# Performance work log

Measured on AMD Instinct MI355X. Metric: run time of the kernel, lower is better.

Reference implementation:

```python
import jax, jax.numpy as jnp
import numpy as np

DIM, NH = 256, 8
B, L_INNER, L_LEAF, L_ROOT = 16, 128, 64, 16


def mha(q, k, v, wi, bi, wo, bo, nh=NH):
    # Faithful torch.nn.MultiheadAttention (batch_first): packed in_proj, q scaled by head_dim**-0.5.
    E = q.shape[-1]
    hd = E // nh
    wq, wk, wv = wi[:E], wi[E:2 * E], wi[2 * E:]
    bq, bk, bv = bi[:E], bi[E:2 * E], bi[2 * E:]

    def proj(x, w, b):
        Bx, Lx, _ = x.shape
        return (x @ w.T + b).reshape(Bx, Lx, nh, hd).transpose(0, 2, 1, 3)  # [B,H,L,hd]

    qh = proj(q, wq, bq) * (float(hd) ** -0.5)
    kh = proj(k, wk, bk)
    vh = proj(v, wv, bv)
    attn = jax.nn.softmax(jnp.einsum('bhqd,bhkd->bhqk', qh, kh), axis=-1)
    o = jnp.einsum('bhqk,bhkd->bhqd', attn, vh).transpose(0, 2, 1, 3).reshape(q.shape)
    return o @ wo.T + bo


def setup_inputs() -> dict:
    key = jax.random.key(0)
    ks = jax.random.split(key, 10)
    return {
        'leaf': jax.random.normal(ks[0], (B * L_INNER, L_LEAF, DIM), jnp.float32),
        'inner': jax.random.normal(ks[1], (B, L_INNER, DIM), jnp.float32),
        'root': jax.random.normal(ks[2], (B, L_ROOT, DIM), jnp.float32),
        'w_in': jax.random.normal(ks[3], (7, 3 * DIM, DIM), jnp.float32) * 0.02,
        'b_in': jax.random.normal(ks[4], (7, 3 * DIM), jnp.float32) * 0.02,
        'w_out': jax.random.normal(ks[5], (7, DIM, DIM), jnp.float32) * 0.02,
        'b_out': jax.random.normal(ks[6], (7, DIM), jnp.float32) * 0.02,
        'weight_leaf': jax.random.normal(ks[7], (2,), jnp.float32),
        'weight_inner': jax.random.normal(ks[8], (3,), jnp.float32),
        'weight_root': jax.random.normal(ks[9], (2,), jnp.float32),
    }


def reference(leaf, inner, root, w_in, b_in, w_out, b_out, weight_leaf, weight_inner, weight_root):
    # param slots: 0 leaf_parents, 1 leaf_siblings, 2 inner_parents, 3 inner_siblings,
    #              4 inner_children, 5 root_siblings, 6 root_children (constructed but UNUSED, as in source)
    inner_flat = inner.reshape(-1, 1, DIM)  # [B*L_inner, 1, dim]

    leaf_p = mha(leaf, inner_flat, inner_flat, w_in[0], b_in[0], w_out[0], b_out[0])
    leaf_s = mha(leaf, leaf, leaf, w_in[1], b_in[1], w_out[1], b_out[1])
    wl = jax.nn.softmax(weight_leaf)
    leaf_out = wl[0] * leaf_p + wl[1] * leaf_s

    inner_p = mha(inner, root, root, w_in[2], b_in[2], w_out[2], b_out[2])
    inner_s = mha(inner, inner, inner, w_in[3], b_in[3], w_out[3], b_out[3])
    inner_c = mha(inner_flat, leaf, leaf, w_in[4], b_in[4], w_out[4], b_out[4]).reshape(inner.shape)
    wi_ = jax.nn.softmax(weight_inner)
    inner_out = wi_[0] * inner_p + wi_[1] * inner_s + wi_[2] * inner_c

    root_s = mha(root, root, root, w_in[5], b_in[5], w_out[5], b_out[5])
    # source bug reproduced: root_c also uses attn_root_siblings (slot 5)
    root_c = mha(root, inner, inner, w_in[5], b_in[5], w_out[5], b_out[5])
    wr = jax.nn.softmax(weight_root)
    root_out = wr[0] * root_s + wr[1] * root_c

    return (leaf_out, inner_out, root_out)
```

## Files before the change

kernel.cpp:

```cpp
#include <hip/hip_runtime.h>
#include <hip/hip_bf16.h>
#include <cstdint>


#define DIM 256
#define NH 8
#define HD 32

static constexpr float SCALE = 0.17677669529663687f;

typedef __bf16 bf16x8 __attribute__((ext_vector_type(8)));
typedef __bf16 bf16x4 __attribute__((ext_vector_type(4)));
typedef float  f32x4  __attribute__((ext_vector_type(4)));

__device__ __forceinline__ float dot4(const float4 a, const float4 b) {
    return a.x * b.x + a.y * b.y + a.z * b.z + a.w * b.w;
}

__device__ __forceinline__ void cvt_range(const float* __restrict__ s,
                                          __bf16* __restrict__ d, int lb, int n) {
    int i = (lb * 256 + (int)threadIdx.x) * 4;
    if (i < n) {
        float4 v = *(const float4*)(s + i);
        d[i + 0] = (__bf16)v.x; d[i + 1] = (__bf16)v.y;
        d[i + 2] = (__bf16)v.z; d[i + 3] = (__bf16)v.w;
    }
}

__global__ __launch_bounds__(256) void cvt_all(
    const float* __restrict__ w_in, const float* __restrict__ w_out,
    __bf16* __restrict__ W1b, __bf16* __restrict__ W4kvb,
    __bf16* __restrict__ Wo1b, __bf16* __restrict__ Wv0b,
    __bf16* __restrict__ Wo0b)
{
    const size_t WI = 768 * 256, WO = 256 * 256;
    const int bid = blockIdx.x;
    if (bid < 192)       cvt_range(w_in + 1 * WI, W1b, bid, 768 * 256);
    else if (bid < 320)  cvt_range(w_in + 4 * WI + 256 * 256, W4kvb, bid - 192, 512 * 256);
    else if (bid < 384)  cvt_range(w_out + 1 * WO, Wo1b, bid - 320, 256 * 256);
    else if (bid < 448)  cvt_range(w_in + 512 * 256, Wv0b, bid - 384, 256 * 256);
    else                 cvt_range(w_out, Wo0b, bid - 448, 256 * 256);
}

__device__ void mega2_body(int g,
    const float* __restrict__ X, const float* __restrict__ inner,
    const __bf16* __restrict__ W1b, const float* __restrict__ Bi1,
    const __bf16* __restrict__ W4kvb, const float* __restrict__ W4q,
    const float* __restrict__ Bi4, __bf16* __restrict__ O1,
    float* __restrict__ Oc, char* __restrict__ smem)
{
    const int xcd  = g & 7;
    const int idx  = g >> 3;
    const int b    = xcd * 256 + (idx >> 2);
    const int hg   = idx & 3;
    const int tid  = threadIdx.x;
    const int wid  = tid >> 6;
    const int lane = tid & 63;
    const int lr   = lane & 15;
    const int lk   = (lane >> 4) * 8;
    const int prow = (lane >> 4) * 4;

    __bf16* Xs  = (__bf16*)smem;
    __bf16* Qs  = (__bf16*)smem;
    __bf16* Pw  = (__bf16*)(smem + wid * 2304);
    __bf16* Ks  = (__bf16*)(smem + 9216);
    __bf16* K4t = (__bf16*)(smem + 18432);
    float* qpart = (float*)(smem + 27648);
    float* qv    = qpart + 256;
    float* psm   = qv + 64;
    float* opart = psm + 128;
    __bf16* Vt  = (__bf16*)(smem + 33792);
    __bf16* V4t = (__bf16*)(smem + 43008);

    {
        const float* xb = X + (size_t)b * 64 * DIM;
#pragma unroll
        for (int it = 0; it < 16; ++it) {
            const int e4 = it * 1024 + tid * 4;
            const f32x4 v = __builtin_nontemporal_load((const f32x4*)(xb + e4));
            bf16x4 t4;
            t4[0] = (__bf16)v[0]; t4[1] = (__bf16)v[1];
            t4[2] = (__bf16)v[2]; t4[3] = (__bf16)v[3];
            const int row = e4 >> 8, col = e4 & 255;
            *(bf16x4*)(Xs + row * 264 + col) = t4;
        }
    }
    __syncthreads();

    bf16x8 af[4][8];
#pragma unroll
    for (int tg = 0; tg < 4; ++tg)
#pragma unroll
        for (int kk = 0; kk < 8; ++kk)
            af[tg][kk] = *(const bf16x8*)(Xs + (size_t)(tg * 16 + lr) * 264 + kk * 32 + lk);
    __syncthreads();

    {
        auto wsrc = [&](int t) -> const __bf16* {
            if (t < 12) {
                const int sec = t >> 2, sub = t & 3;
                return W1b + (size_t)(sec * 256 + hg * 64 + sub * 16) * DIM;
            }
            const int u = t - 12, sec = u >> 2, sub = u & 3;
            return W4kvb + (size_t)(sec * 256 + hg * 64 + sub * 16) * DIM;
        };
        const size_t boff = (size_t)lr * DIM + lk;
        const int t0w = wid * 5;
        bf16x8 bw[8], bn[8];
        {
            const __bf16* p = wsrc(t0w) + boff;
#pragma unroll
            for (int kk = 0; kk < 8; ++kk) bw[kk] = *(const bf16x8*)(p + kk * 32);
        }
        for (int i = 0; i < 5; ++i) {
            const int t = t0w + i;
            if (i + 1 < 5) {
                const __bf16* p = wsrc(t + 1) + boff;
#pragma unroll
                for (int kk = 0; kk < 8; ++kk) bn[kk] = *(const bf16x8*)(p + kk * 32);
            }
            f32x4 acc0 = {0.f,0.f,0.f,0.f}, acc1 = {0.f,0.f,0.f,0.f};
            f32x4 acc2 = {0.f,0.f,0.f,0.f}, acc3 = {0.f,0.f,0.f,0.f};
#pragma unroll
            for (int kk = 0; kk < 8; ++kk) {
                acc0 = __builtin_amdgcn_mfma_f32_16x16x32_bf16(af[0][kk], bw[kk], acc0, 0, 0, 0);
                acc1 = __builtin_amdgcn_mfma_f32_16x16x32_bf16(af[1][kk], bw[kk], acc1, 0, 0, 0);
                acc2 = __builtin_amdgcn_mfma_f32_16x16x32_bf16(af[2][kk], bw[kk], acc2, 0, 0, 0);
                acc3 = __builtin_amdgcn_mfma_f32_16x16x32_bf16(af[3][kk], bw[kk], acc3, 0, 0, 0);
            }
            f32x4 accT[4] = { acc0, acc1, acc2, acc3 };
            const int sub = t & 3;
            const int col = sub * 16 + lr;
            if (t < 4) {
                const float bias = Bi1[hg * 64 + sub * 16 + lr];
#pragma unroll
                for (int tg = 0; tg < 4; ++tg)
#pragma unroll
                    for (int r = 0; r < 4; ++r)
                        Qs[(size_t)(tg * 16 + prow + r) * 72 + col] =
                            (__bf16)((accT[tg][r] + bias) * SCALE);
            } else if (t < 8) {
                const float bias = Bi1[256 + hg * 64 + sub * 16 + lr];
#pragma unroll
                for (int tg = 0; tg < 4; ++tg)
#pragma unroll
                    for (int r = 0; r < 4; ++r)
                        Ks[(size_t)(tg * 16 + prow + r) * 72 + col] =
                            (__bf16)(accT[tg][r] + bias);
            } else if (t < 12) {
                const float bias = Bi1[512 + hg * 64 + sub * 16 + lr];
#pragma unroll
                for (int tg = 0; tg < 4; ++tg) {
                    bf16x4 pv;
#pragma unroll
                    for (int r = 0; r < 4; ++r) pv[r] = (__bf16)(accT[tg][r] + bias);
                    *(bf16x4*)(Vt + (size_t)col * 72 + tg * 16 + prow) = pv;
                }
            } else if (t < 16) {
                const float bias = Bi4[256 + hg * 64 + sub * 16 + lr];
#pragma unroll
                for (int tg = 0; tg < 4; ++tg) {
                    bf16x4 pv;
#pragma unroll
                    for (int r = 0; r < 4; ++r) pv[r] = (__bf16)(accT[tg][r] + bias);
                    *(bf16x4*)(K4t + (size_t)col * 72 + tg * 16 + prow) = pv;
                }
            } else {
                const float bias = Bi4[512 + hg * 64 + sub * 16 + lr];
#pragma unroll
                for (int tg = 0; tg < 4; ++tg) {
                    bf16x4 pv;
#pragma unroll
                    for (int r = 0; r < 4; ++r) pv[r] = (__bf16)(accT[tg][r] + bias);
                    *(bf16x4*)(V4t + (size_t)col * 72 + tg * 16 + prow) = pv;
                }
            }
#pragma unroll
            for (int kk = 0; kk < 8; ++kk) bw[kk] = bn[kk];
        }
    }
    __syncthreads();

    {
        const int o = tid & 63, part = tid >> 6;
        const float4* wr = (const float4*)(W4q + (size_t)(hg * 64 + o) * DIM + part * 64);
        const float4* xr = (const float4*)(inner + (size_t)b * DIM + part * 64);
        float accq = 0.f;
#pragma unroll
        for (int k = 0; k < 16; ++k) accq += dot4(xr[k], wr[k]);
        qpart[part * 64 + o] = accq;
    }
    __syncthreads();

    if (tid < 64)
        qv[tid] = (qpart[tid] + qpart[64 + tid] + qpart[128 + tid] + qpart[192 + tid]
                   + Bi4[hg * 64 + tid]) * SCALE;

    const int hh = wid >> 1;
    const int qh = wid & 1;
    f32x4 s[2][4];
    {
        bf16x8 kb[4];
#pragma unroll
        for (int kt = 0; kt < 4; ++kt)
            kb[kt] = *(const bf16x8*)(Ks + (size_t)(kt * 16 + lr) * 72 + hh * 32 + lk);
#pragma unroll
        for (int q2 = 0; q2 < 2; ++q2) {
            const int qt = qh * 2 + q2;
            const bf16x8 qa = *(const bf16x8*)(Qs + (size_t)(qt * 16 + lr) * 72 + hh * 32 + lk);
#pragma unroll
            for (int kt = 0; kt < 4; ++kt) {
                f32x4 z = {0.f, 0.f, 0.f, 0.f};
                s[q2][kt] = __builtin_amdgcn_mfma_f32_16x16x32_bf16(qa, kb[kt], z, 0, 0, 0);
            }
        }
    }
#pragma unroll
    for (int q2 = 0; q2 < 2; ++q2) {
#pragma unroll
        for (int r = 0; r < 4; ++r) {
            float m = fmaxf(fmaxf(s[q2][0][r], s[q2][1][r]), fmaxf(s[q2][2][r], s[q2][3][r]));
#pragma unroll
            for (int off = 1; off < 16; off <<= 1) m = fmaxf(m, __shfl_xor(m, off));
            const float p0 = __expf(s[q2][0][r] - m), p1 = __expf(s[q2][1][r] - m);
            const float p2 = __expf(s[q2][2][r] - m), p3 = __expf(s[q2][3][r] - m);
            float t = p0 + p1 + p2 + p3;
#pragma unroll
            for (int off = 1; off < 16; off <<= 1) t += __shfl_xor(t, off);
            const float inv = 1.0f / t;
            s[q2][0][r] = p0 * inv; s[q2][1][r] = p1 * inv;
            s[q2][2][r] = p2 * inv; s[q2][3][r] = p3 * inv;
        }
    }
    bf16x8 vb[2][2];
#pragma unroll
    for (int dt = 0; dt < 2; ++dt)
#pragma unroll
        for (int ks = 0; ks < 2; ++ks)
            vb[dt][ks] = *(const bf16x8*)(Vt + (size_t)(hh * 32 + dt * 16 + lr) * 72 + ks * 32 + lk);
    __syncthreads();

    {
#pragma unroll
        for (int q2 = 0; q2 < 2; ++q2) {
            const int qt = qh * 2 + q2;
#pragma unroll
            for (int kt = 0; kt < 4; ++kt)
#pragma unroll
                for (int r = 0; r < 4; ++r)
                    Pw[(size_t)(prow + r) * 72 + kt * 16 + lr] = (__bf16)s[q2][kt][r];
            bf16x8 pa[2];
#pragma unroll
            for (int ks = 0; ks < 2; ++ks)
                pa[ks] = *(const bf16x8*)(Pw + (size_t)lr * 72 + ks * 32 + lk);
#pragma unroll
            for (int dt = 0; dt < 2; ++dt) {
                f32x4 o = {0.f, 0.f, 0.f, 0.f};
#pragma unroll
                for (int ks = 0; ks < 2; ++ks)
                    o = __builtin_amdgcn_mfma_f32_16x16x32_bf16(pa[ks], vb[dt][ks], o, 0, 0, 0);
                const int colO = (hg * 2 + hh) * 32 + dt * 16 + lr;
#pragma unroll
                for (int r = 0; r < 4; ++r)
                    __builtin_nontemporal_store((__bf16)o[r],
                        &O1[((size_t)b * 64 + qt * 16 + prow + r) * DIM + colO]);
            }
        }
    }
    __syncthreads();

    if (wid < 2) {
        const int j = lane;
        float sv = 0.f;
#pragma unroll
        for (int d = 0; d < 32; ++d)
            sv += qv[wid * 32 + d] * (float)K4t[(size_t)(wid * 32 + d) * 72 + j];
        float m = sv;
#pragma unroll
        for (int off = 1; off < 64; off <<= 1) m = fmaxf(m, __shfl_xor(m, off));
        const float p = __expf(sv - m);
        float t = p;
#pragma unroll
        for (int off = 1; off < 64; off <<= 1) t += __shfl_xor(t, off);
        psm[wid * 64 + j] = p / t;
    }
    __syncthreads();

    if (tid < 128) {
        const int o = tid & 63, hf = tid >> 6;
        const int ho = o >> 5;
        float acc2 = 0.f;
#pragma unroll
        for (int j = 0; j < 32; ++j)
            acc2 += psm[ho * 64 + hf * 32 + j] * (float)V4t[(size_t)o * 72 + hf * 32 + j];
        opart[hf * 64 + o] = acc2;
    }
    __syncthreads();
    if (tid < 64)
        Oc[(size_t)b * DIM + hg * 64 + tid] = opart[tid] + opart[64 + tid];
}

__device__ void leafp_mfma_body(int bid, const float* __restrict__ inner,
    const __bf16* __restrict__ Wv0b, const __bf16* __restrict__ Wo0b,
    const float* __restrict__ b_in0, const float* __restrict__ b_out0,
    float* __restrict__ tP, char* __restrict__ smem)
{
    __bf16* tV = (__bf16*)smem;
    __bf16* Bs = (__bf16*)(smem + 33792);
    const int tid  = threadIdx.x;
    const int wid  = tid >> 6;
    const int lane = tid & 63;
    const int lr   = lane & 15;
    const int lk   = (lane >> 4) * 8;
    const int prow = (lane >> 4) * 4;
    const int tok0 = wid * 16 + prow;
    const int srow = tid >> 5;
    const int scol = (tid & 31) * 8;

    bf16x8 a[8];
    {
        const float* xrow = inner + ((size_t)bid * 64 + wid * 16 + lr) * DIM + lk;
#pragma unroll
        for (int k = 0; k < 8; ++k) {
            float4 v0 = *(const float4*)(xrow + k * 32);
            float4 v1 = *(const float4*)(xrow + k * 32 + 4);
            bf16x8 t;
            t[0] = (__bf16)v0.x; t[1] = (__bf16)v0.y; t[2] = (__bf16)v0.z; t[3] = (__bf16)v0.w;
            t[4] = (__bf16)v1.x; t[5] = (__bf16)v1.y; t[6] = (__bf16)v1.z; t[7] = (__bf16)v1.w;
            a[k] = t;
        }
    }

    {
        bf16x8 g0 = *(const bf16x8*)(Wv0b + (size_t)srow * DIM + scol);
        bf16x8 g1 = *(const bf16x8*)(Wv0b + (size_t)(8 + srow) * DIM + scol);
        *(bf16x8*)(Bs + srow * 264 + scol) = g0;
        *(bf16x8*)(Bs + (8 + srow) * 264 + scol) = g1;
    }
    __syncthreads();
    for (int t = 0; t < 16; ++t) {
        const int cur = t & 1;
        const __bf16* Bc = Bs + cur * 4224;
        bf16x8 g0, g1;
        if (t + 1 < 16) {
            const __bf16* p = Wv0b + (size_t)((t + 1) * 16) * DIM;
            g0 = *(const bf16x8*)(p + (size_t)srow * DIM + scol);
            g1 = *(const bf16x8*)(p + (size_t)(8 + srow) * DIM + scol);
        }
        f32x4 acc = {0.f, 0.f, 0.f, 0.f};
#pragma unroll
        for (int k = 0; k < 8; ++k)
            acc = __builtin_amdgcn_mfma_f32_16x16x32_bf16(
                a[k], *(const bf16x8*)(Bc + lr * 264 + k * 32 + lk), acc, 0, 0, 0);
        const float bias = b_in0[512 + t * 16 + lr];
#pragma unroll
        for (int r = 0; r < 4; ++r)
            tV[(size_t)(tok0 + r) * 264 + t * 16 + lr] = (__bf16)(acc[r] + bias);
        if (t + 1 < 16) {
            __bf16* Bn = Bs + (cur ^ 1) * 4224;
            *(bf16x8*)(Bn + srow * 264 + scol) = g0;
            *(bf16x8*)(Bn + (8 + srow) * 264 + scol) = g1;
        }
        __syncthreads();
    }

    bf16x8 a2[8];
#pragma unroll
    for (int k = 0; k < 8; ++k)
        a2[k] = *(const bf16x8*)(tV + (size_t)(wid * 16 + lr) * 264 + k * 32 + lk);
    {
        bf16x8 g0 = *(const bf16x8*)(Wo0b + (size_t)srow * DIM + scol);
        bf16x8 g1 = *(const bf16x8*)(Wo0b + (size_t)(8 + srow) * DIM + scol);
        *(bf16x8*)(Bs + srow * 264 + scol) = g0;
        *(bf16x8*)(Bs + (8 + srow) * 264 + scol) = g1;
    }
    __syncthreads();
    for (int t = 0; t < 16; ++t) {
        const int cur = t & 1;
        const __bf16* Bc = Bs + cur * 4224;
        bf16x8 g0, g1;
        if (t + 1 < 16) {
            const __bf16* p = Wo0b + (size_t)((t + 1) * 16) * DIM;
            g0 = *(const bf16x8*)(p + (size_t)srow * DIM + scol);
            g1 = *(const bf16x8*)(p + (size_t)(8 + srow) * DIM + scol);
        }
        f32x4 acc = {0.f, 0.f, 0.f, 0.f};
#pragma unroll
        for (int k = 0; k < 8; ++k)
            acc = __builtin_amdgcn_mfma_f32_16x16x32_bf16(
                a2[k], *(const bf16x8*)(Bc + lr * 264 + k * 32 + lk), acc, 0, 0, 0);
        const float bo = b_out0[t * 16 + lr];
#pragma unroll
        for (int r = 0; r < 4; ++r)
            tP[((size_t)bid * 64 + wid * 16 + prow + r) * DIM + t * 16 + lr] = acc[r] + bo;
        if (t + 1 < 16) {
            __bf16* Bn = Bs + (cur ^ 1) * 4224;
            *(bf16x8*)(Bn + srow * 264 + scol) = g0;
            *(bf16x8*)(Bn + (8 + srow) * 264 + scol) = g1;
        }
        __syncthreads();
    }
}

template <int LQ, int LK, int RQ>
__device__ void attn_body(int bx, const float* __restrict__ Xq,
                          const float* __restrict__ Xkv,
                          const float* __restrict__ Wi, const float* __restrict__ Bi,
                          float* __restrict__ O, float* __restrict__ sm)
{
    const int b   = bx >> 3;
    const int h   = bx & 7;
    const int tid = threadIdx.x;

    float* KsP = sm;
    float* VsP = KsP + LK * 33;
    float* QsP = VsP + LK * 33;
    float* SP  = QsP + RQ * 33;

    const float* xq  = Xq  + (size_t)b * LQ * DIM;
    const float* xkv = Xkv + (size_t)b * LK * DIM;

    {
        const int col   = tid & 63;
        const int which = col >> 5;
        const int d     = col & 31;
        const int row   = DIM + which * DIM + h * HD + d;
        const float4* wr = (const float4*)(Wi + (size_t)row * DIM);
        const float bias = Bi[row];
        constexpr int TT = LK / 4;
        float acc[TT];
#pragma unroll
        for (int i = 0; i < TT; ++i) acc[i] = 0.f;
        const int t0 = tid >> 6;
        for (int k4 = 0; k4 < DIM / 4; ++k4) {
            const float4 w = wr[k4];
#pragma unroll
            for (int i = 0; i < TT; ++i) {
                const int t = t0 + 4 * i;
                const float4 aa = ((const float4*)(xkv + (size_t)t * DIM))[k4];
                acc[i] += dot4(aa, w);
            }
        }
#pragma unroll
        for (int i = 0; i < TT; ++i) {
            const int t = t0 + 4 * i;
            if (which == 0) KsP[t * 33 + d] = acc[i] + bias;
            else            VsP[t * 33 + d] = acc[i] + bias;
        }
    }
    __syncthreads();

    for (int q0 = 0; q0 < LQ; q0 += RQ) {
        {
            const int d  = tid & 31;
            const int rg = tid >> 5;
            const int row = h * HD + d;
            const float4* wr = (const float4*)(Wi + (size_t)row * DIM);
            const float bias = Bi[row];
#pragma unroll
            for (int i = 0; i < RQ / 8; ++i) {
                const int rloc = rg + 8 * i;
                float acc = 0.f;
                const float4* xr = (const float4*)(xq + (size_t)(q0 + rloc) * DIM);
                for (int k4 = 0; k4 < DIM / 4; ++k4) acc += dot4(xr[k4], wr[k4]);
                QsP[rloc * 33 + d] = (acc + bias) * SCALE;
            }
        }
        __syncthreads();
        for (int idx = tid; idx < RQ * LK; idx += 256) {
            const int r = idx / LK;
            const int j = idx - r * LK;
            float acc = 0.f;
#pragma unroll
            for (int d = 0; d < HD; ++d)
                acc += QsP[r * 33 + d] * KsP[j * 33 + d];
            SP[r * (LK + 1) + j] = acc;
        }
        __syncthreads();
        if (tid < RQ * 8) {
            const int r   = tid >> 3;
            const int sub = tid & 7;
            float m = -1e30f;
            for (int j = sub; j < LK; j += 8) m = fmaxf(m, SP[r * (LK + 1) + j]);
#pragma unroll
            for (int off = 4; off; off >>= 1) m = fmaxf(m, __shfl_xor(m, off, 8));
            float sum = 0.f;
            for (int j = sub; j < LK; j += 8) {
                const float p = __expf(SP[r * (LK + 1) + j] - m);
                SP[r * (LK + 1) + j] = p;
                sum += p;
            }
#pragma unroll
            for (int off = 4; off; off >>= 1) sum += __shfl_xor(sum, off, 8);
            const float inv = 1.0f / sum;
            for (int j = sub; j < LK; j += 8) SP[r * (LK + 1) + j] *= inv;
        }
        __syncthreads();
        for (int idx = tid; idx < RQ * HD; idx += 256) {
            const int r = idx >> 5;
            const int d = idx & 31;
            float acc = 0.f;
            for (int j = 0; j < LK; ++j)
                acc += SP[r * (LK + 1) + j] * VsP[j * 33 + d];
            O[((size_t)(b * LQ + q0 + r)) * DIM + h * HD + d] = acc;
        }
        __syncthreads();
    }
}

__global__ __launch_bounds__(256) void fused_main(
    const float* __restrict__ leaf, const float* __restrict__ inner,
    const float* __restrict__ root,
    const float* __restrict__ w_in, const float* __restrict__ b_in,
    const float* __restrict__ b_out,
    const __bf16* __restrict__ W1b, const __bf16* __restrict__ W4kvb,
    const __bf16* __restrict__ Wv0b, const __bf16* __restrict__ Wo0b,
    __bf16* __restrict__ O1, float* __restrict__ Oc, float* __restrict__ tP,
    float* __restrict__ Op, float* __restrict__ Osf,
    float* __restrict__ Ors, float* __restrict__ Orc)
{
    extern __shared__ __align__(16) char smem[];
    const int bid = blockIdx.x;
    const size_t WI = 768 * 256, BI = 768;
    if (bid < 128)
        attn_body<128, 128, 16>(bid, inner, inner, w_in + 3 * WI, b_in + 3 * BI,
                                Osf, (float*)smem);
    else if (bid < 256)
        attn_body<128, 16, 32>(bid - 128, inner, root, w_in + 2 * WI, b_in + 2 * BI,
                               Op, (float*)smem);
    else if (bid < 384)
        attn_body<16, 128, 16>(bid - 256, root, inner, w_in + 5 * WI, b_in + 5 * BI,
                               Orc, (float*)smem);
    else if (bid < 512)
        attn_body<16, 16, 16>(bid - 384, root, root, w_in + 5 * WI, b_in + 5 * BI,
                              Ors, (float*)smem);
    else if (bid < 544)
        leafp_mfma_body(bid - 512, inner, Wv0b, Wo0b, b_in, b_out, tP, smem);
    else
        mega2_body(bid - 544, leaf, inner, W1b, b_in + 1 * BI, W4kvb,
                   w_in + 4 * WI, b_in + 4 * BI, O1, Oc, smem);
}

__device__ void combleaf_body(int bid, const __bf16* __restrict__ O1,
    const __bf16* __restrict__ Wo1, const float* __restrict__ Bo1,
    const float* __restrict__ tP, const float* __restrict__ wleaf,
    float* __restrict__ out, char* __restrict__ smem)
{
    __bf16* Ws = (__bf16*)smem;
    const int tid  = threadIdx.x;
    const int wid  = tid >> 6;
    const int lane = tid & 63;
    const int lr   = lane & 15;
    const int lk   = (lane >> 4) * 8;
    const int prow = (lane >> 4) * 4;

    bf16x8 a[4][8];
#pragma unroll
    for (int tg = 0; tg < 4; ++tg) {
        const __bf16* ar = O1 + ((size_t)bid * 512 + wid * 64 + tg * 16 + lr) * DIM + lk;
#pragma unroll
        for (int k = 0; k < 8; ++k) a[tg][k] = *(const bf16x8*)(ar + k * 32);
    }
    {
        const int row = tid >> 1, hf = tid & 1;
        const __bf16* p = Wo1 + (size_t)row * DIM + hf * 128;
        __bf16* dst = Ws + (size_t)row * 264 + hf * 128;
#pragma unroll
        for (int q = 0; q < 16; ++q)
            *(bf16x8*)(dst + q * 8) = *(const bf16x8*)(p + q * 8);
    }
    __syncthreads();

    const float e0 = __expf(wleaf[0]), e1 = __expf(wleaf[1]);
    const float wl0 = e0 / (e0 + e1), wl1 = e1 / (e0 + e1);
    const int   tile = bid * 8 + wid;
    const size_t rb  = (size_t)bid * 512 + wid * 64;

    for (int nt = 0; nt < 16; ++nt) {
        bf16x8 bw[8];
#pragma unroll
        for (int k = 0; k < 8; ++k)
            bw[k] = *(const bf16x8*)(Ws + (size_t)(nt * 16 + lr) * 264 + k * 32 + lk);
        f32x4 acc0 = {0.f,0.f,0.f,0.f}, acc1 = {0.f,0.f,0.f,0.f};
        f32x4 acc2 = {0.f,0.f,0.f,0.f}, acc3 = {0.f,0.f,0.f,0.f};
#pragma unroll
        for (int k = 0; k < 8; ++k) {
            acc0 = __builtin_amdgcn_mfma_f32_16x16x32_bf16(a[0][k], bw[k], acc0, 0, 0, 0);
            acc1 = __builtin_amdgcn_mfma_f32_16x16x32_bf16(a[1][k], bw[k], acc1, 0, 0, 0);
            acc2 = __builtin_amdgcn_mfma_f32_16x16x32_bf16(a[2][k], bw[k], acc2, 0, 0, 0);
            acc3 = __builtin_amdgcn_mfma_f32_16x16x32_bf16(a[3][k], bw[k], acc3, 0, 0, 0);
        }
        f32x4 accT[4] = { acc0, acc1, acc2, acc3 };
        const int   o  = nt * 16 + lr;
        const float bo = Bo1[o];
        const float tv = tP[(size_t)tile * DIM + o];
#pragma unroll
        for (int tg = 0; tg < 4; ++tg)
#pragma unroll
            for (int r = 0; r < 4; ++r)
                out[(rb + tg * 16 + prow + r) * DIM + o] =
                    wl0 * tv + wl1 * (accT[tg][r] + bo);
    }
}

__device__ void combine_inner_body(int vb, const float* __restrict__ Op,
    const float* __restrict__ Osf, const float* __restrict__ Oc,
    const float* __restrict__ W2, const float* __restrict__ B2,
    const float* __restrict__ W3, const float* __restrict__ B3,
    const float* __restrict__ W4, const float* __restrict__ B4,
    const float* __restrict__ winner, float* __restrict__ out, float* __restrict__ Ts)
{
    const int n0 = vb * 32;
    const int o  = threadIdx.x & 255;
    const float e0 = __expf(winner[0]), e1 = __expf(winner[1]), e2 = __expf(winner[2]);
    const float inv = 1.f / (e0 + e1 + e2);
    const float wt0 = e0 * inv, wt1 = e1 * inv, wt2 = e2 * inv;

    float acc[32];
#pragma unroll
    for (int r = 0; r < 32; ++r) acc[r] = 0.f;
    const float biasacc = wt0 * B2[o] + wt1 * B3[o] + wt2 * B4[o];

#pragma unroll
    for (int term = 0; term < 3; ++term) {
        const float* Ob = (term == 0) ? Op : (term == 1) ? Osf : Oc;
        const float* Wb = (term == 0) ? W2 : (term == 1) ? W3 : W4;
        const float wt  = (term == 0) ? wt0 : (term == 1) ? wt1 : wt2;
        __syncthreads();
        for (int idx = threadIdx.x; idx < 32 * DIM; idx += 256)
            Ts[idx] = Ob[(size_t)n0 * DIM + idx];
        __syncthreads();
        const float4* wr = (const float4*)(Wb + (size_t)o * DIM);
        for (int k4 = 0; k4 < DIM / 4; ++k4) {
            float4 w = wr[k4];
            w.x *= wt; w.y *= wt; w.z *= wt; w.w *= wt;
#pragma unroll
            for (int r = 0; r < 32; ++r) {
                const float4 aa = *(const float4*)&Ts[r * DIM + k4 * 4];
                acc[r] += dot4(aa, w);
            }
        }
    }
#pragma unroll
    for (int r = 0; r < 32; ++r)
        out[(size_t)(n0 + r) * DIM + o] = acc[r] + biasacc;
}

__device__ void combine_root_body(int vb, const float* __restrict__ Ors,
    const float* __restrict__ Orc, const float* __restrict__ W5,
    const float* __restrict__ B5, const float* __restrict__ wroot,
    float* __restrict__ out, float* __restrict__ Ts)
{
    const int n0 = vb * 32;
    const int o  = threadIdx.x & 255;
    const float e0 = __expf(wroot[0]), e1 = __expf(wroot[1]);
    const float w0 = e0 / (e0 + e1), w1 = e1 / (e0 + e1);
    for (int idx = threadIdx.x; idx < 32 * DIM; idx += 256)
        Ts[idx] = w0 * Ors[(size_t)n0 * DIM + idx] + w1 * Orc[(size_t)n0 * DIM + idx];
    __syncthreads();
    float acc[32];
#pragma unroll
    for (int r = 0; r < 32; ++r) acc[r] = 0.f;
    const float4* wr = (const float4*)(W5 + (size_t)o * DIM);
    for (int k4 = 0; k4 < DIM / 4; ++k4) {
        const float4 w = wr[k4];
#pragma unroll
        for (int r = 0; r < 32; ++r) {
            const float4 aa = *(const float4*)&Ts[r * DIM + k4 * 4];
            acc[r] += dot4(aa, w);
        }
    }
    const float bo = B5[o];
#pragma unroll
    for (int r = 0; r < 32; ++r)
        out[(size_t)(n0 + r) * DIM + o] = acc[r] + bo;
}

__global__ __launch_bounds__(512) void epilogue_kernel(
    const __bf16* __restrict__ O1, const __bf16* __restrict__ Wo1b,
    const float* __restrict__ w_out, const float* __restrict__ b_out,
    const float* __restrict__ tP, const float* __restrict__ Op,
    const float* __restrict__ Osf, const float* __restrict__ Oc,
    const float* __restrict__ Ors, const float* __restrict__ Orc,
    const float* __restrict__ wleaf, const float* __restrict__ winner,
    const float* __restrict__ wroot, float* __restrict__ out)
{
    extern __shared__ __align__(16) char smem[];
    const int bid = blockIdx.x;
    const size_t WO = 256 * 256, BO = 256;
    if (bid < 256) {
        combleaf_body(bid, O1, Wo1b, b_out + BO, tP, wleaf, out, smem);
    } else if (bid < 320) {
        if (threadIdx.x < 256)
            combine_inner_body(bid - 256, Op, Osf, Oc,
                               w_out + 2 * WO, b_out + 2 * BO,
                               w_out + 3 * WO, b_out + 3 * BO,
                               w_out + 4 * WO, b_out + 4 * BO,
                               winner, out + 33554432, (float*)smem);
        else {
#pragma unroll
            for (int i = 0; i < 6; ++i) __syncthreads();
        }
    } else {
        if (threadIdx.x < 256)
            combine_root_body(bid - 320, Ors, Orc, w_out + 5 * WO, b_out + 5 * BO,
                              wroot, out + 33554432 + 524288, (float*)smem);
        else
            __syncthreads();
    }
}

extern "C" void kernel_launch(void* const* d_in, const int* in_sizes, int n_in,
                              void* d_out, int out_size, void* d_ws, size_t ws_size,
                              hipStream_t stream)
{
    const float* leaf   = (const float*)d_in[0];
    const float* inner  = (const float*)d_in[1];
    const float* root   = (const float*)d_in[2];
    const float* w_in   = (const float*)d_in[3];
    const float* b_in   = (const float*)d_in[4];
    const float* w_out  = (const float*)d_in[5];
    const float* b_out  = (const float*)d_in[6];
    const float* wleaf  = (const float*)d_in[7];
    const float* winner = (const float*)d_in[8];
    const float* wroot  = (const float*)d_in[9];
    float* out = (float*)d_out;

    char* ws = (char*)d_ws;
    __bf16* W1b   = (__bf16*)(ws);
    __bf16* W4kvb = (__bf16*)(ws + 393216);
    __bf16* Wo1b  = (__bf16*)(ws + 655360);
    __bf16* Wv0b  = (__bf16*)(ws + 786432);
    __bf16* Wo0b  = (__bf16*)(ws + 917504);
    __bf16* O1b   = (__bf16*)(ws + 1048576);
    float*  tP    = (float*)(ws + 68157440);
    float*  Oc    = (float*)(ws + 70254592);
    float*  Op    = (float*)(ws + 72351744);
    float*  Osf   = (float*)(ws + 74448896);
    float*  Ors   = (float*)(ws + 76546048);
    float*  Orc   = (float*)(ws + 76808192);

    cvt_all<<<512, 256, 0, stream>>>(w_in, w_out, W1b, W4kvb, Wo1b, Wv0b, Wo0b);

    fused_main<<<8736, 256, 52224, stream>>>(
        leaf, inner, root, w_in, b_in, b_out, W1b, W4kvb, Wv0b, Wo0b,
        O1b, Oc, tP, Op, Osf, Ors, Orc);

    epilogue_kernel<<<328, 512, 135168, stream>>>(O1b, Wo1b, w_out, b_out, tP,
                                                  Op, Osf, Oc, Ors, Orc,
                                                  wleaf, winner, wroot, out);
}
```

Before: 768.7 us.

## De-alias shared memory buffers to drop barriers and batch Q projection

Gives the leaf-block kernel separate LDS regions for Q/K/V/K4/V4 instead of overlaying them on the X staging area. This lets two __syncthreads be removed: one after loading A fragments and one before the P·V stage. In attn_body, the Q projection for all query rows now runs once up front, with register-blocked accumulation, instead of once per RQ chunk inside the loop, which removes a barrier per chunk. Dynamic shared memory grows from 52KB to about 80KB and launch_bounds asks for 2 blocks per CU. Each block uses more LDS, which may cut residency.

```diff
diff --git a/kernel.cpp b/kernel.cpp
--- a/kernel.cpp
+++ b/kernel.cpp
@@ -61,16 +61,16 @@
     const int prow = (lane >> 4) * 4;
 
     __bf16* Xs  = (__bf16*)smem;
-    __bf16* Qs  = (__bf16*)smem;
     __bf16* Pw  = (__bf16*)(smem + wid * 2304);
-    __bf16* Ks  = (__bf16*)(smem + 9216);
-    __bf16* K4t = (__bf16*)(smem + 18432);
-    float* qpart = (float*)(smem + 27648);
+    float* qpart = (float*)(smem + 9216);
     float* qv    = qpart + 256;
     float* psm   = qv + 64;
     float* opart = psm + 128;
-    __bf16* Vt  = (__bf16*)(smem + 33792);
-    __bf16* V4t = (__bf16*)(smem + 43008);
+    __bf16* Qs  = (__bf16*)(smem + 33792);
+    __bf16* Ks  = (__bf16*)(smem + 43008);
+    __bf16* Vt  = (__bf16*)(smem + 52224);
+    __bf16* K4t = (__bf16*)(smem + 61440);
+    __bf16* V4t = (__bf16*)(smem + 70656);
 
     {
         const float* xb = X + (size_t)b * 64 * DIM;
@@ -93,7 +93,6 @@
 #pragma unroll
         for (int kk = 0; kk < 8; ++kk)
             af[tg][kk] = *(const bf16x8*)(Xs + (size_t)(tg * 16 + lr) * 264 + kk * 32 + lk);
-    __syncthreads();
 
     {
         auto wsrc = [&](int t) -> const __bf16* {
@@ -232,15 +231,13 @@
             s[q2][2][r] = p2 * inv; s[q2][3][r] = p3 * inv;
         }
     }
-    bf16x8 vb[2][2];
-#pragma unroll
-    for (int dt = 0; dt < 2; ++dt)
-#pragma unroll
-        for (int ks = 0; ks < 2; ++ks)
-            vb[dt][ks] = *(const bf16x8*)(Vt + (size_t)(hh * 32 + dt * 16 + lr) * 72 + ks * 32 + lk);
-    __syncthreads();
-
-    {
+    {
+        bf16x8 vb[2][2];
+#pragma unroll
+        for (int dt = 0; dt < 2; ++dt)
+#pragma unroll
+            for (int ks = 0; ks < 2; ++ks)
+                vb[dt][ks] = *(const bf16x8*)(Vt + (size_t)(hh * 32 + dt * 16 + lr) * 72 + ks * 32 + lk);
 #pragma unroll
         for (int q2 = 0; q2 < 2; ++q2) {
             const int qt = qh * 2 + q2;
@@ -415,7 +412,7 @@
     float* KsP = sm;
     float* VsP = KsP + LK * 33;
     float* QsP = VsP + LK * 33;
-    float* SP  = QsP + RQ * 33;
+    float* SP  = QsP + LQ * 33;
 
     const float* xq  = Xq  + (size_t)b * LQ * DIM;
     const float* xkv = Xkv + (size_t)b * LK * DIM;
@@ -448,32 +445,44 @@
             else            VsP[t * 33 + d] = acc[i] + bias;
         }
     }
-    __syncthreads();
-
-    for (int q0 = 0; q0 < LQ; q0 += RQ) {
-        {
-            const int d  = tid & 31;
-            const int rg = tid >> 5;
+    {
+        constexpr int TGQ = (LQ >= 8) ? 8 : LQ;
+        constexpr int TT  = LQ / TGQ;
+        if (tid < 32 * TGQ) {
+            const int d   = tid & 31;
             const int row = h * HD + d;
             const float4* wr = (const float4*)(Wi + (size_t)row * DIM);
             const float bias = Bi[row];
-#pragma unroll
-            for (int i = 0; i < RQ / 8; ++i) {
-                const int rloc = rg + 8 * i;
-                float acc = 0.f;
-                const float4* xr = (const float4*)(xq + (size_t)(q0 + rloc) * DIM);
-                for (int k4 = 0; k4 < DIM / 4; ++k4) acc += dot4(xr[k4], wr[k4]);
-                QsP[rloc * 33 + d] = (acc + bias) * SCALE;
-            }
-        }
-        __syncthreads();
+            float acc[TT];
+#pragma unroll
+            for (int i = 0; i < TT; ++i) acc[i] = 0.f;
+            const int t0 = tid >> 5;
+            for (int k4 = 0; k4 < DIM / 4; ++k4) {
+                const float4 w = wr[k4];
+#pragma unroll
+                for (int i = 0; i < TT; ++i) {
+                    const int t = t0 + TGQ * i;
+                    const float4 aa = ((const float4*)(xq + (size_t)t * DIM))[k4];
+                    acc[i] += dot4(aa, w);
+                }
+            }
+#pragma unroll
+            for (int i = 0; i < TT; ++i) {
+                const int t = t0 + TGQ * i;
+                QsP[t * 33 + d] = (acc[i] + bias) * SCALE;
+            }
+        }
+    }
+    __syncthreads();
+
+    for (int q0 = 0; q0 < LQ; q0 += RQ) {
         for (int idx = tid; idx < RQ * LK; idx += 256) {
             const int r = idx / LK;
             const int j = idx - r * LK;
             float acc = 0.f;
 #pragma unroll
             for (int d = 0; d < HD; ++d)
-                acc += QsP[r * 33 + d] * KsP[j * 33 + d];
+                acc += QsP[(q0 + r) * 33 + d] * KsP[j * 33 + d];
             SP[r * (LK + 1) + j] = acc;
         }
         __syncthreads();
@@ -508,7 +517,7 @@
     }
 }
 
-__global__ __launch_bounds__(256) void fused_main(
+__global__ __launch_bounds__(256, 2) void fused_main(
     const float* __restrict__ leaf, const float* __restrict__ inner,
     const float* __restrict__ root,
     const float* __restrict__ w_in, const float* __restrict__ b_in,
@@ -742,7 +751,7 @@
 
     cvt_all<<<512, 256, 0, stream>>>(w_in, w_out, W1b, W4kvb, Wo1b, Wv0b, Wo0b);
 
-    fused_main<<<8736, 256, 52224, stream>>>(
+    fused_main<<<8736, 256, 79872, stream>>>(
         leaf, inner, root, w_in, b_in, b_out, W1b, W4kvb, Wv0b, Wo0b,
         O1b, Oc, tP, Op, Osf, Ors, Orc);
 
```

Result: faster. 660.3 us, median of 2 (-14.1%).
